# Kernel tuning notes

Measured on AMD Instinct MI355X. Metric: run time of the kernel, lower is better.

## Reference

```python
import jax, jax.numpy as jnp
import numpy as np
from jax import lax

B, MID, OUT, H, W = 16, 128, 512, 112, 112
EPS = 1e-5


def _conv(x, w, stride=1, pad=0, dil=1, groups=1):
    return lax.conv_general_dilated(
        x, w, window_strides=(stride, stride),
        padding=[(pad, pad), (pad, pad)], rhs_dilation=(dil, dil),
        feature_group_count=groups,
        dimension_numbers=('NCHW', 'OIHW', 'NCHW'))


def setup_inputs() -> dict:
    key = jax.random.key(0)
    ks = jax.random.split(key, 12)
    s = 0.05
    return {
        'x': jax.random.normal(ks[0], (B, 2 * MID, H, W), jnp.float32),
        # kernel_gen: Linear(mid, mid*9, bias=False) weight [mid*9, mid]
        'W_kg': jax.random.normal(ks[1], (MID * 9, MID), jnp.float32) * s,
        # global stream: depthwise 3x3 dil=2, then 1x1 conv, BN
        'gdw_w': jax.random.normal(ks[2], (MID, 1, 3, 3), jnp.float32) * s,
        'gdw_b': jax.random.normal(ks[3], (MID,), jnp.float32) * s,
        'gpw_w': jax.random.normal(ks[4], (MID, MID, 1, 1), jnp.float32) * s,
        'gpw_b': jax.random.normal(ks[5], (MID,), jnp.float32) * s,
        'bn1_g': jnp.ones((MID,), jnp.float32),
        'bn1_b': jnp.zeros((MID,), jnp.float32),
        'bn1_m': jax.random.normal(ks[6], (MID,), jnp.float32) * s,
        'bn1_v': jax.random.uniform(ks[7], (MID,), jnp.float32, 0.5, 1.5),
        # downsample: Conv2d(2*mid, out, 3, stride=2, pad=1), BN
        'ds_w': jax.random.normal(ks[8], (OUT, 2 * MID, 3, 3), jnp.float32) * s,
        'ds_b': jax.random.normal(ks[9], (OUT,), jnp.float32) * s,
        'bn2_g': jnp.ones((OUT,), jnp.float32),
        'bn2_b': jnp.zeros((OUT,), jnp.float32),
        'bn2_m': jax.random.normal(ks[10], (OUT,), jnp.float32) * s,
        'bn2_v': jax.random.uniform(ks[11], (OUT,), jnp.float32, 0.5, 1.5),
    }


def _bn(x, g, b, m, v):  # eval-mode BatchNorm2d
    inv = g / jnp.sqrt(v + EPS)
    return x * inv[None, :, None, None] + (b - m * inv)[None, :, None, None]


def reference(x, W_kg, gdw_w, gdw_b, gpw_w, gpw_b,
              bn1_g, bn1_b, bn1_m, bn1_v,
              ds_w, ds_b, bn2_g, bn2_b, bn2_m, bn2_v):
    local_in, global_in = jnp.split(x, 2, axis=1)  # [B,MID,H,W] each
    b, c, h, w = local_in.shape

    # local branch: pool -> linear+relu kernel-gen -> per-sample depthwise 3x3
    pooled = jnp.mean(local_in, axis=(2, 3))                  # [b,c]
    kernels = jax.nn.relu(pooled @ W_kg.T)                    # [b, c*9]
    kernels = kernels.reshape(b * c, 1, 3, 3)
    local_out = _conv(local_in.reshape(1, b * c, h, w), kernels,
                      pad=1, groups=b * c).reshape(b, c, h, w)

    # global branch: depthwise dil-2 conv -> 1x1 conv -> BN -> ReLU
    g = _conv(global_in, gdw_w, pad=2, dil=2, groups=c) + gdw_b[None, :, None, None]
    g = _conv(g, gpw_w) + gpw_b[None, :, None, None]
    g = jax.nn.relu(_bn(g, bn1_g, bn1_b, bn1_m, bn1_v))

    combined = jnp.concatenate([local_out, g], axis=1)        # [b,2c,h,w]
    out = _conv(combined, ds_w, stride=2, pad=1) + ds_b[None, :, None, None]
    out = jax.nn.relu(_bn(out, bn2_g, bn2_b, bn2_m, bn2_v))   # [b,OUT,h/2,w/2]
    return out
```

## Files before the change

kernel.cpp:

```cpp
#include <hip/hip_runtime.h>


#define DEVI static __device__ __forceinline__

using bf16x8 = __attribute__((ext_vector_type(8))) short;
using f32x4  = __attribute__((ext_vector_type(4))) float;
typedef unsigned short ushort_t;

constexpr int Bn = 16, MID = 128, CHN = 256, Hh = 112, Wn = 112;
constexpr int OHn = 56, OWn = 56, OCn = 512;
constexpr int HW  = Hh * Wn;
constexpr int KDS = CHN * 9;
constexpr float EPSf = 1e-5f;

constexpr size_t C_I = 56 * 64;
constexpr size_t C_P = 4 * C_I;
constexpr size_t C_H = 2 * C_P;
constexpr size_t C_B = (size_t)Hh * C_H;

DEVI ushort_t f2b(float f) {
    unsigned u = __float_as_uint(f);
    return (ushort_t)((u + 0x7FFFu + ((u >> 16) & 1u)) >> 16);
}
DEVI float b2f(ushort_t s) { return __uint_as_float(((unsigned)s) << 16); }

DEVI void gl_lds16(const void* g, void* l) {
    __builtin_amdgcn_global_load_lds(
        (const __attribute__((address_space(1))) unsigned int*)g,
        (__attribute__((address_space(3))) unsigned int*)l, 16, 0, 0);
}

__global__ __launch_bounds__(256) void k_prep(
        const float* __restrict__ gpw_w, const float* __restrict__ gpw_b,
        const float* __restrict__ bn1g, const float* __restrict__ bn1b,
        const float* __restrict__ bn1m, const float* __restrict__ bn1v,
        const float* __restrict__ dsb,
        const float* __restrict__ bn2g, const float* __restrict__ bn2b,
        const float* __restrict__ bn2m, const float* __restrict__ bn2v,
        ushort_t* __restrict__ gpwbf,
        float* __restrict__ a1, float* __restrict__ b1,
        float* __restrict__ a2, float* __restrict__ b2,
        float* __restrict__ pooled) {
    int i = blockIdx.x * 256 + threadIdx.x;
    if (i < MID * MID) gpwbf[i] = f2b(gpw_w[i]);
    if (i < Bn * MID) pooled[i] = 0.f;
    if (i < OCn) {
        float inv = bn2g[i] / sqrtf(bn2v[i] + EPSf);
        a2[i] = inv;
        b2[i] = bn2b[i] + (dsb[i] - bn2m[i]) * inv;
    }
    if (i < MID) {
        float inv = bn1g[i] / sqrtf(bn1v[i] + EPSf);
        a1[i] = inv;
        b1[i] = bn1b[i] + (gpw_b[i] - bn1m[i]) * inv;
    }
}

__global__ __launch_bounds__(256) void k_wds(const float* __restrict__ dsw,
                                             ushort_t* __restrict__ wds2) {
    int d = blockIdx.x * 256 + threadIdx.x;
    int j = d & 63, oc = (d >> 6) & 511, kb = d >> 15;
    int khw = kb >> 2, icc = kb & 3;
    int ph = j >> 3, c = ph ^ (oc & 7);
    int ic = icc * 64 + c * 8 + (j & 7);
    wds2[d] = f2b(dsw[((size_t)oc * CHN + ic) * 9 + khw]);
}

__global__ __launch_bounds__(256) void k_kgen(const float* __restrict__ pooled,
                                              const float* __restrict__ wkg,
                                              float* __restrict__ kgen) {
    int idx = blockIdx.x * 256 + threadIdx.x;
    int b = idx / 1152, j = idx % 1152;
    const float* pr = pooled + b * MID;
    const float* wr = wkg + (size_t)j * MID;
    float s = 0.f;
#pragma unroll 8
    for (int i = 0; i < MID; i++) s += pr[i] * wr[i];
    kgen[idx] = fmaxf(s * (1.f / HW), 0.f);
}

__global__ __launch_bounds__(256) void k_xt(const float* __restrict__ x,
                                            ushort_t* __restrict__ xT,
                                            float* __restrict__ pooled) {
    __shared__ ushort_t tile[Wn * 264];
    int t = threadIdx.x;
    int bh = blockIdx.x;
    int b = bh / Hh, h = bh % Hh;
    const float* xp = x + ((size_t)b * CHN * Hh + h) * Wn;
    for (int idx = t; idx < CHN * 28; idx += 256) {
        int ch = idx / 28, q = idx % 28;
        float4 v = *(const float4*)(xp + (size_t)ch * HW + q * 4);
        int w = q * 4;
        tile[w * 264 + ch]       = f2b(v.x);
        tile[(w + 1) * 264 + ch] = f2b(v.y);
        tile[(w + 2) * 264 + ch] = f2b(v.z);
        tile[(w + 3) * 264 + ch] = f2b(v.w);
    }
    __syncthreads();
    int4* dst = (int4*)(xT + (size_t)bh * Wn * CHN);
    for (int q = t; q < Wn * CHN / 8; q += 256) {
        int w = q >> 5, c0 = (q & 31) << 3;
        dst[q] = *(const int4*)(tile + w * 264 + c0);
    }
    if (t < MID) {
        float s = 0.f;
        for (int w = 0; w < Wn; w++) s += b2f(tile[w * 264 + t]);
        atomicAdd(&pooled[b * MID + t], s);
    }
}

__global__ __launch_bounds__(256) void k_dwc(
        const ushort_t* __restrict__ xT, const float* __restrict__ kgen,
        const float* __restrict__ gdw_w, const float* __restrict__ gdw_b,
        const ushort_t* __restrict__ gpwbf,
        const float* __restrict__ a1, const float* __restrict__ b1,
        ushort_t* __restrict__ comb) {
    __shared__ float wtab[1152];
    __shared__ ushort_t pbuf[112 * 136];
    int t = threadIdx.x;
    int h  = blockIdx.x;
    int by = blockIdx.y;
    int b = by >> 1, br = by & 1;
    const float* wg = br ? gdw_w : (kgen + b * 1152);
    {
        const float4* src = (const float4*)wg;
        float4* dstw = (float4*)wtab;
        dstw[t] = src[t];
        if (t < 32) dstw[256 + t] = src[256 + t];
    }
    __syncthreads();
    int cg = t & 15, wlane = t >> 4;
    int c0 = cg << 3;
    float wk[9][8];
#pragma unroll
    for (int tp = 0; tp < 9; tp++)
#pragma unroll
        for (int k = 0; k < 8; k++)
            wk[tp][k] = wtab[(c0 + k) * 9 + tp];
    float bias[8] = {0.f, 0.f, 0.f, 0.f, 0.f, 0.f, 0.f, 0.f};
    if (br) {
        *(float4*)&bias[0] = *(const float4*)(gdw_b + c0);
        *(float4*)&bias[4] = *(const float4*)(gdw_b + c0 + 4);
    }
    const ushort_t* xb = xT + (size_t)b * HW * CHN + (br ? MID : 0) + c0;
    int dil = 1 + br;
    for (int ws = 0; ws < 7; ws++) {
        int w = ws * 16 + wlane;
        float acc[8];
#pragma unroll
        for (int k = 0; k < 8; k++) acc[k] = bias[k];
#pragma unroll
        for (int dh = -1; dh <= 1; dh++) {
            int h1 = h + dh * dil;
            if ((unsigned)h1 >= (unsigned)Hh) continue;
#pragma unroll
            for (int dw = -1; dw <= 1; dw++) {
                int w1 = w + dw * dil;
                if ((unsigned)w1 >= (unsigned)Wn) continue;
                union { int4 v; ushort_t u[8]; } U;
                U.v = *(const int4*)(xb + (size_t)(h1 * Wn + w1) * CHN);
                int tp = (dh + 1) * 3 + (dw + 1);
#pragma unroll
                for (int k = 0; k < 8; k++)
                    acc[k] += wk[tp][k] * b2f(U.u[k]);
            }
        }
        union { int4 v; ushort_t u[8]; } O;
#pragma unroll
        for (int k = 0; k < 8; k++) O.u[k] = f2b(acc[k]);
        if (br == 0) {
            int w2 = w >> 1, p = w & 1;
            int icc = c0 >> 6, cch = (c0 & 63) >> 3, ph = cch ^ (w2 & 7);
            *(int4*)(comb + (size_t)b * C_B + (size_t)h * C_H + p * C_P
                     + icc * C_I + w2 * 64 + ph * 8) = O.v;
        } else {
            int ph = cg ^ wlane;
            *(int4*)(pbuf + (size_t)w * 128 + ph * 8) = O.v;
        }
    }
    if (br == 0) return;
    __syncthreads();
    int lane = t & 63, wave = t >> 6;
    int mrow = lane & 15, quad = lane >> 4;
    const short* gw = (const short*)gpwbf;
    f32x4 acc2[7][2] = {};
#pragma unroll
    for (int ks = 0; ks < 4; ks++) {
        bf16x8 bfr[2];
#pragma unroll
        for (int n = 0; n < 2; n++)
            bfr[n] = *(const bf16x8*)(gw + (size_t)(wave * 32 + n * 16 + mrow) * MID
                                         + ks * 32 + quad * 8);
#pragma unroll
        for (int m = 0; m < 7; m++) {
            int ph = (ks * 4 + quad) ^ mrow;
            bf16x8 af = *(const bf16x8*)(pbuf + (size_t)(m * 16 + mrow) * 128 + ph * 8);
#pragma unroll
            for (int n = 0; n < 2; n++)
                acc2[m][n] = __builtin_amdgcn_mfma_f32_16x16x32_bf16(
                    af, bfr[n], acc2[m][n], 0, 0, 0);
        }
    }
    __syncthreads();
#pragma unroll
    for (int m = 0; m < 7; m++)
#pragma unroll
        for (int n = 0; n < 2; n++) {
            int oc2 = wave * 32 + n * 16 + mrow;
            float al = a1[oc2], be = b1[oc2];
#pragma unroll
            for (int r = 0; r < 4; r++) {
                int px = m * 16 + quad * 4 + r;
                pbuf[px * 136 + oc2] = f2b(fmaxf(acc2[m][n][r] * al + be, 0.f));
            }
        }
    __syncthreads();
    for (int ws = 0; ws < 7; ws++) {
        int w = ws * 16 + wlane;
        int4 v = *(const int4*)(pbuf + (size_t)w * 136 + c0);
        int w2 = w >> 1, p = w & 1;
        int gch = MID + c0;
        int icc = gch >> 6, cch = (gch & 63) >> 3, ph = cch ^ (w2 & 7);
        *(int4*)(comb + (size_t)b * C_B + (size_t)h * C_H + p * C_P
                 + icc * C_I + w2 * 64 + ph * 8) = v;
    }
}

__global__ __launch_bounds__(256) void k_ds(
        const ushort_t* __restrict__ comb, const ushort_t* __restrict__ wds2,
        const float* __restrict__ a2, const float* __restrict__ b2,
        float* __restrict__ out) {
    __shared__ ushort_t lA[128 * 64];
    __shared__ ushort_t lB[128 * 64];
    int t = threadIdx.x, lane = t & 63, wave = t >> 6;
    int g = blockIdx.x;
    int xcd = g & 7, s = g >> 3;
    int octile = s & 3, pl = s >> 2;
    int pair = xcd * 56 + pl;
    int bb = pair / 28, ohp = pair % 28;
    int oh0 = ohp * 2, oc0 = octile * 128;
    int mrow = lane & 15, quad = lane >> 4;
    int wm = wave & 1, wn = wave >> 1;
    int ak = mrow & 7;

    f32x4 acc[4][4] = {};
    for (int kt = 0; kt < 36; kt++) {
        int khw = kt >> 2, icc = kt & 3;
        int kh = khw / 3, kw = khw - kh * 3;
        int p = (kw == 1) ? 0 : 1;
        bool zh0 = (oh0 == 0) && (kh == 0);
        int ldsShift = (kw == 0) ? 128 : 0;
        __syncthreads();
        if (zh0) {
            int4 z = {0, 0, 0, 0};
            *(int4*)(lB + t * 8) = z;
            *(int4*)(lB + 2048 + t * 8) = z;
        }
        if (kw == 0 && t < 16) {
            int4 z = {0, 0, 0, 0};
            *(int4*)(lB + (t >> 3) * 4096 + (t & 7) * 8) = z;
        }
        const char* asrc = (const char*)wds2
            + ((size_t)kt * 32768 + (size_t)oc0 * 64) * 2 + lane * 16;
#pragma unroll
        for (int i = 0; i < 4; i++) {
            int j = wave * 4 + i;
            gl_lds16(asrc + j * 1024, (char*)lA + j * 1024);
        }
        for (int j = wave; j < 14; j += 4) {
            int osub = (j >= 7) ? 1 : 0, jj = j - osub * 7;
            if (zh0 && osub == 0) continue;
            int r = 2 * oh0 + 2 * osub + kh - 1;
            const char* bsrc = (const char*)comb
                + ((size_t)bb * C_B + (size_t)r * C_H + (size_t)p * C_P
                   + (size_t)icc * C_I) * 2 + jj * 1024 + lane * 16;
            gl_lds16(bsrc, (char*)lB + osub * 8192 + ldsShift + jj * 1024);
        }
        __syncthreads();
        int bk = (mrow + ((kw == 0) ? 7 : 0)) & 7;
#pragma unroll
        for (int ks = 0; ks < 2; ks++) {
            bf16x8 af[4], bf[4];
#pragma unroll
            for (int m = 0; m < 4; m++) {
                int row = wm * 64 + m * 16 + mrow;
                int ph = (ks * 4 + quad) ^ ak;
                af[m] = *(const bf16x8*)(lA + row * 64 + ph * 8);
            }
#pragma unroll
            for (int n = 0; n < 4; n++) {
                int nr = wn * 64 + n * 16 + mrow;
                int ph = (ks * 4 + quad) ^ bk;
                bf[n] = *(const bf16x8*)(lB + nr * 64 + ph * 8);
            }
#pragma unroll
            for (int m = 0; m < 4; m++)
#pragma unroll
                for (int n = 0; n < 4; n++)
                    acc[m][n] = __builtin_amdgcn_mfma_f32_16x16x32_bf16(
                        af[m], bf[n], acc[m][n], 0, 0, 0);
        }
    }
#pragma unroll
    for (int m = 0; m < 4; m++) {
#pragma unroll
        for (int r4 = 0; r4 < 4; r4++) {
            int oc = oc0 + wm * 64 + m * 16 + quad * 4 + r4;
            float al = a2[oc], be = b2[oc];
#pragma unroll
            for (int n = 0; n < 4; n++) {
                int nr = wn * 64 + n * 16 + mrow;
                int osub = nr >> 6, ow = nr & 63;
                if (ow < OWn) {
                    float v = fmaxf(acc[m][n][r4] * al + be, 0.f);
                    out[((size_t)(bb * OCn + oc) * OHn + (oh0 + osub)) * OWn + ow] = v;
                }
            }
        }
    }
}

extern "C" void kernel_launch(void* const* d_in, const int* in_sizes, int n_in,
                              void* d_out, int out_size, void* d_ws, size_t ws_size,
                              hipStream_t stream) {
    const float* x     = (const float*)d_in[0];
    const float* wkg   = (const float*)d_in[1];
    const float* gdw_w = (const float*)d_in[2];
    const float* gdw_b = (const float*)d_in[3];
    const float* gpw_w = (const float*)d_in[4];
    const float* gpw_b = (const float*)d_in[5];
    const float* bn1g  = (const float*)d_in[6];
    const float* bn1b  = (const float*)d_in[7];
    const float* bn1m  = (const float*)d_in[8];
    const float* bn1v  = (const float*)d_in[9];
    const float* dsw   = (const float*)d_in[10];
    const float* dsb   = (const float*)d_in[11];
    const float* bn2g  = (const float*)d_in[12];
    const float* bn2b  = (const float*)d_in[13];
    const float* bn2m  = (const float*)d_in[14];
    const float* bn2v  = (const float*)d_in[15];

    char* ws = (char*)d_ws;
    float*    pooled = (float*)(ws + 0);
    float*    kgen   = (float*)(ws + 8192);
    float*    a1     = (float*)(ws + 81920);
    float*    b1     = (float*)(ws + 82432);
    float*    a2     = (float*)(ws + 82944);
    float*    b2     = (float*)(ws + 84992);
    ushort_t* gpwbf  = (ushort_t*)(ws + 87040);
    ushort_t* wds2   = (ushort_t*)(ws + 119808);
    ushort_t* comb   = (ushort_t*)(ws + 2479104);
    ushort_t* xT  = (ushort_t*)d_out;
    float*    out = (float*)d_out;

    k_prep<<<64, 256, 0, stream>>>(gpw_w, gpw_b, bn1g, bn1b, bn1m, bn1v,
                                   dsb, bn2g, bn2b, bn2m, bn2v,
                                   gpwbf, a1, b1, a2, b2, pooled);
    k_wds <<<4608, 256, 0, stream>>>(dsw, wds2);
    k_xt  <<<1792, 256, 0, stream>>>(x, xT, pooled);
    k_kgen<<<72, 256, 0, stream>>>(pooled, wkg, kgen);
    k_dwc <<<dim3(Hh, Bn * 2), 256, 0, stream>>>(xT, kgen, gdw_w, gdw_b,
                                                 gpwbf, a1, b1, comb);
    k_ds  <<<1792, 256, 0, stream>>>(comb, wds2, a2, b2, out);
}
```

Baseline: 415.8 us.

## Split depthwise kernel into local/global kernels with register sliding-window reuse

Splits the combined depthwise kernel into two kernels, one for the local branch and one for the global branch, so each drops the runtime dilation branching. Each thread now computes 7 contiguous output columns and loads the input row once into registers as a sliding window, instead of reloading 9 taps per output. The kernel-gen output and the weight tables are re-laid out tap-major so weights load as float4 vectors. The cost is higher register pressure (56 accumulators plus the window), an extra kernel launch, and different pbuf swizzle indexing.

```diff
diff --git a/kernel.cpp b/kernel.cpp
--- a/kernel.cpp
+++ b/kernel.cpp
@@ -10,7 +10,6 @@
 constexpr int Bn = 16, MID = 128, CHN = 256, Hh = 112, Wn = 112;
 constexpr int OHn = 56, OWn = 56, OCn = 512;
 constexpr int HW  = Hh * Wn;
-constexpr int KDS = CHN * 9;
 constexpr float EPSf = 1e-5f;
 
 constexpr size_t C_I = 56 * 64;
@@ -23,6 +22,9 @@
     return (ushort_t)((u + 0x7FFFu + ((u >> 16) & 1u)) >> 16);
 }
 DEVI float b2f(ushort_t s) { return __uint_as_float(((unsigned)s) << 16); }
+DEVI int pack2(float a, float b) {
+    return (int)f2b(a) | ((int)f2b(b) << 16);
+}
 
 DEVI void gl_lds16(const void* g, void* l) {
     __builtin_amdgcn_global_load_lds(
@@ -71,8 +73,9 @@
                                               float* __restrict__ kgen) {
     int idx = blockIdx.x * 256 + threadIdx.x;
     int b = idx / 1152, j = idx % 1152;
+    int c = j & 127, tp = j >> 7;
     const float* pr = pooled + b * MID;
-    const float* wr = wkg + (size_t)j * MID;
+    const float* wr = wkg + (size_t)(c * 9 + tp) * MID;
     float s = 0.f;
 #pragma unroll 8
     for (int i = 0; i < MID; i++) s += pr[i] * wr[i];
@@ -109,8 +112,93 @@
     }
 }
 
-__global__ __launch_bounds__(256) void k_dwc(
+template <int DIL>
+DEVI void dw_accum_row(const ushort_t* __restrict__ rp,
+                       const float* __restrict__ wtab, int tb,
+                       int c0, int wbase, float (&acc)[7][8]) {
+    constexpr int NC = 7 + 2 * DIL;
+    float wk[3][8];
+#pragma unroll
+    for (int dw = 0; dw < 3; dw++) {
+        float4 lo = *(const float4*)&wtab[(tb + dw) * 128 + c0];
+        float4 hi = *(const float4*)&wtab[(tb + dw) * 128 + c0 + 4];
+        wk[dw][0] = lo.x; wk[dw][1] = lo.y; wk[dw][2] = lo.z; wk[dw][3] = lo.w;
+        wk[dw][4] = hi.x; wk[dw][5] = hi.y; wk[dw][6] = hi.z; wk[dw][7] = hi.w;
+    }
+    int4 C[NC];
+#pragma unroll
+    for (int j = 0; j < NC; j++) {
+        int w1 = wbase - DIL + j;
+        int4 v = make_int4(0, 0, 0, 0);
+        if ((unsigned)w1 < (unsigned)Wn)
+            v = *(const int4*)(rp + (size_t)w1 * CHN);
+        C[j] = v;
+    }
+#pragma unroll
+    for (int j = 0; j < NC; j++) {
+        float f[8];
+        {
+            unsigned u;
+            u = (unsigned)C[j].x;
+            f[0] = __uint_as_float(u << 16); f[1] = __uint_as_float(u & 0xffff0000u);
+            u = (unsigned)C[j].y;
+            f[2] = __uint_as_float(u << 16); f[3] = __uint_as_float(u & 0xffff0000u);
+            u = (unsigned)C[j].z;
+            f[4] = __uint_as_float(u << 16); f[5] = __uint_as_float(u & 0xffff0000u);
+            u = (unsigned)C[j].w;
+            f[6] = __uint_as_float(u << 16); f[7] = __uint_as_float(u & 0xffff0000u);
+        }
+#pragma unroll
+        for (int dw = 0; dw < 3; dw++) {
+            int i = j - dw * DIL;
+            if (i >= 0 && i <= 6) {
+#pragma unroll
+                for (int k = 0; k < 8; k++) acc[i][k] += wk[dw][k] * f[k];
+            }
+        }
+    }
+}
+
+__global__ __launch_bounds__(256, 3) void k_dwl(
         const ushort_t* __restrict__ xT, const float* __restrict__ kgen,
+        ushort_t* __restrict__ comb) {
+    __shared__ float wtab[1152];
+    int t = threadIdx.x;
+    int h = blockIdx.x, b = blockIdx.y;
+    {
+        const float4* src = (const float4*)(kgen + (size_t)b * 1152);
+        float4* dstw = (float4*)wtab;
+        dstw[t] = src[t];
+        if (t < 32) dstw[256 + t] = src[256 + t];
+    }
+    __syncthreads();
+    int cg = t & 15, wl = t >> 4, c0 = cg << 3, wbase = 7 * wl;
+    const ushort_t* xb = xT + (size_t)b * HW * CHN + c0;
+    float acc[7][8] = {};
+#pragma unroll
+    for (int dh = -1; dh <= 1; dh++) {
+        int h1 = h + dh;
+        if ((unsigned)h1 >= (unsigned)Hh) continue;
+        dw_accum_row<1>(xb + (size_t)h1 * Wn * CHN, wtab, (dh + 1) * 3,
+                        c0, wbase, acc);
+    }
+    int icc = c0 >> 6, cch = (c0 & 63) >> 3;
+#pragma unroll
+    for (int i = 0; i < 7; i++) {
+        int w = wbase + i;
+        int4 O;
+        O.x = pack2(acc[i][0], acc[i][1]);
+        O.y = pack2(acc[i][2], acc[i][3]);
+        O.z = pack2(acc[i][4], acc[i][5]);
+        O.w = pack2(acc[i][6], acc[i][7]);
+        int w2 = w >> 1, p = w & 1, ph = cch ^ (w2 & 7);
+        *(int4*)(comb + (size_t)b * C_B + (size_t)h * C_H + p * C_P
+                 + icc * C_I + w2 * 64 + ph * 8) = O;
+    }
+}
+
+__global__ __launch_bounds__(256, 3) void k_dwg(
+        const ushort_t* __restrict__ xT,
         const float* __restrict__ gdw_w, const float* __restrict__ gdw_b,
         const ushort_t* __restrict__ gpwbf,
         const float* __restrict__ a1, const float* __restrict__ b1,
@@ -118,67 +206,46 @@
     __shared__ float wtab[1152];
     __shared__ ushort_t pbuf[112 * 136];
     int t = threadIdx.x;
-    int h  = blockIdx.x;
-    int by = blockIdx.y;
-    int b = by >> 1, br = by & 1;
-    const float* wg = br ? gdw_w : (kgen + b * 1152);
+    int h = blockIdx.x, b = blockIdx.y;
+    for (int e4 = t; e4 < 288; e4 += 256) {
+        float4 v = *(const float4*)(gdw_w + (size_t)e4 * 4);
+        int e = e4 * 4;
+        wtab[(e % 9) * 128 + e / 9]             = v.x;
+        wtab[((e + 1) % 9) * 128 + (e + 1) / 9] = v.y;
+        wtab[((e + 2) % 9) * 128 + (e + 2) / 9] = v.z;
+        wtab[((e + 3) % 9) * 128 + (e + 3) / 9] = v.w;
+    }
+    __syncthreads();
+    int cg = t & 15, wl = t >> 4, c0 = cg << 3, wbase = 7 * wl;
+    const ushort_t* xb = xT + (size_t)b * HW * CHN + MID + c0;
+    float acc[7][8];
     {
-        const float4* src = (const float4*)wg;
-        float4* dstw = (float4*)wtab;
-        dstw[t] = src[t];
-        if (t < 32) dstw[256 + t] = src[256 + t];
-    }
-    __syncthreads();
-    int cg = t & 15, wlane = t >> 4;
-    int c0 = cg << 3;
-    float wk[9][8];
-#pragma unroll
-    for (int tp = 0; tp < 9; tp++)
-#pragma unroll
-        for (int k = 0; k < 8; k++)
-            wk[tp][k] = wtab[(c0 + k) * 9 + tp];
-    float bias[8] = {0.f, 0.f, 0.f, 0.f, 0.f, 0.f, 0.f, 0.f};
-    if (br) {
-        *(float4*)&bias[0] = *(const float4*)(gdw_b + c0);
-        *(float4*)&bias[4] = *(const float4*)(gdw_b + c0 + 4);
-    }
-    const ushort_t* xb = xT + (size_t)b * HW * CHN + (br ? MID : 0) + c0;
-    int dil = 1 + br;
-    for (int ws = 0; ws < 7; ws++) {
-        int w = ws * 16 + wlane;
-        float acc[8];
-#pragma unroll
-        for (int k = 0; k < 8; k++) acc[k] = bias[k];
-#pragma unroll
-        for (int dh = -1; dh <= 1; dh++) {
-            int h1 = h + dh * dil;
-            if ((unsigned)h1 >= (unsigned)Hh) continue;
-#pragma unroll
-            for (int dw = -1; dw <= 1; dw++) {
-                int w1 = w + dw * dil;
-                if ((unsigned)w1 >= (unsigned)Wn) continue;
-                union { int4 v; ushort_t u[8]; } U;
-                U.v = *(const int4*)(xb + (size_t)(h1 * Wn + w1) * CHN);
-                int tp = (dh + 1) * 3 + (dw + 1);
-#pragma unroll
-                for (int k = 0; k < 8; k++)
-                    acc[k] += wk[tp][k] * b2f(U.u[k]);
-            }
-        }
-        union { int4 v; ushort_t u[8]; } O;
-#pragma unroll
-        for (int k = 0; k < 8; k++) O.u[k] = f2b(acc[k]);
-        if (br == 0) {
-            int w2 = w >> 1, p = w & 1;
-            int icc = c0 >> 6, cch = (c0 & 63) >> 3, ph = cch ^ (w2 & 7);
-            *(int4*)(comb + (size_t)b * C_B + (size_t)h * C_H + p * C_P
-                     + icc * C_I + w2 * 64 + ph * 8) = O.v;
-        } else {
-            int ph = cg ^ wlane;
-            *(int4*)(pbuf + (size_t)w * 128 + ph * 8) = O.v;
-        }
-    }
-    if (br == 0) return;
+        float4 b0 = *(const float4*)(gdw_b + c0);
+        float4 b4 = *(const float4*)(gdw_b + c0 + 4);
+#pragma unroll
+        for (int i = 0; i < 7; i++) {
+            acc[i][0] = b0.x; acc[i][1] = b0.y; acc[i][2] = b0.z; acc[i][3] = b0.w;
+            acc[i][4] = b4.x; acc[i][5] = b4.y; acc[i][6] = b4.z; acc[i][7] = b4.w;
+        }
+    }
+#pragma unroll
+    for (int dh = -1; dh <= 1; dh++) {
+        int h1 = h + 2 * dh;
+        if ((unsigned)h1 >= (unsigned)Hh) continue;
+        dw_accum_row<2>(xb + (size_t)h1 * Wn * CHN, wtab, (dh + 1) * 3,
+                        c0, wbase, acc);
+    }
+#pragma unroll
+    for (int i = 0; i < 7; i++) {
+        int w = wbase + i;
+        int4 O;
+        O.x = pack2(acc[i][0], acc[i][1]);
+        O.y = pack2(acc[i][2], acc[i][3]);
+        O.z = pack2(acc[i][4], acc[i][5]);
+        O.w = pack2(acc[i][6], acc[i][7]);
+        int ph = cg ^ (w & 15);
+        *(int4*)(pbuf + (size_t)w * 128 + ph * 8) = O;
+    }
     __syncthreads();
     int lane = t & 63, wave = t >> 6;
     int mrow = lane & 15, quad = lane >> 4;
@@ -216,7 +283,7 @@
         }
     __syncthreads();
     for (int ws = 0; ws < 7; ws++) {
-        int w = ws * 16 + wlane;
+        int w = ws * 16 + wl;
         int4 v = *(const int4*)(pbuf + (size_t)w * 136 + c0);
         int w2 = w >> 1, p = w & 1;
         int gch = MID + c0;
@@ -359,7 +426,8 @@
     k_wds <<<4608, 256, 0, stream>>>(dsw, wds2);
     k_xt  <<<1792, 256, 0, stream>>>(x, xT, pooled);
     k_kgen<<<72, 256, 0, stream>>>(pooled, wkg, kgen);
-    k_dwc <<<dim3(Hh, Bn * 2), 256, 0, stream>>>(xT, kgen, gdw_w, gdw_b,
-                                                 gpwbf, a1, b1, comb);
+    k_dwg <<<dim3(Hh, Bn), 256, 0, stream>>>(xT, gdw_w, gdw_b, gpwbf,
+                                             a1, b1, comb);
+    k_dwl <<<dim3(Hh, Bn), 256, 0, stream>>>(xT, kgen, comb);
     k_ds  <<<1792, 256, 0, stream>>>(comb, wds2, a2, b2, out);
 }
```

Result: faster. 339.4 us (-18.4%).
